# Performance work log

Hardware: AMD Instinct MI355X
Metric: run time of the kernel (lower is better)

The kernel has to match this reference:

```python
import jax, jax.numpy as jnp
import numpy as np

ALPHA = 1.0  # args.alpha
BS, N_HIDDEN, N_CLUSTERS = 1048576, 64, 64


def setup_inputs() -> dict:
    key = jax.random.key(0)
    k1, k2 = jax.random.split(key)
    z = jax.random.normal(k1, (BS, N_HIDDEN), dtype=jnp.float32)
    centroids = jax.random.normal(k2, (N_CLUSTERS, N_HIDDEN), dtype=jnp.float32)
    return {"z": z, "centroids": centroids}


def reference(z, centroids):
    # EUC similarity: sim[b,k] = sqrt(sum_h (z[b,h] - c[k,h])^2)
    # computed via ||z||^2 + ||c||^2 - 2 z c^T (same math, no (K,bs,H) blowup)
    z2 = jnp.sum(z * z, axis=1, keepdims=True)            # (bs, 1)
    c2 = jnp.sum(centroids * centroids, axis=1)           # (K,)
    d2 = z2 + c2[None, :] - 2.0 * (z @ centroids.T)       # (bs, K)
    sim = jnp.sqrt(jnp.maximum(d2, 0.0))

    # Student-t soft assignment Q and target distribution P
    Q = (1.0 + sim / ALPHA) ** (-(ALPHA + 1.0) / 2.0)
    Q = Q / jnp.sum(Q, axis=1, keepdims=True)             # row-normalize
    P = (Q * Q) / jnp.sum(Q, axis=0, keepdims=True)       # col-sum sharpen
    P = P / jnp.sum(P, axis=1, keepdims=True)             # row-normalize
    return Q, P
```

## Files before the change

### kernel.cpp

```cpp
#include <hip/hip_runtime.h>

#define BS_N 1048576
#define NH 64
#define NK 64

#define WS_C2_OFF 512

__device__ __forceinline__ float frcp(float x) { return __builtin_amdgcn_rcpf(x); }

__global__ void k0_init(const float* __restrict__ c, float* __restrict__ ws) {
    const int t = threadIdx.x;
    for (int i = t; i < 512; i += 128) ws[i] = 0.f;
    if (t < 64) {
        const float* row = c + t * NH;
        float s0 = 0.f, s1 = 0.f, s2 = 0.f, s3 = 0.f;
#pragma unroll
        for (int h = 0; h < NH; h += 4) {
            s0 = fmaf(row[h + 0], row[h + 0], s0);
            s1 = fmaf(row[h + 1], row[h + 1], s1);
            s2 = fmaf(row[h + 2], row[h + 2], s2);
            s3 = fmaf(row[h + 3], row[h + 3], s3);
        }
        ws[WS_C2_OFF + t] = (s0 + s1) + (s2 + s3);
    }
}

__global__ __launch_bounds__(128) void k1_q(const float* __restrict__ z,
                                            const float* __restrict__ c,
                                            float* __restrict__ ws,
                                            float* __restrict__ Q) {
    __shared__ float qs[128 * 65];
    __shared__ float rs[128];
    __shared__ float cpart[2][64];
    const int t = threadIdx.x;
    const long long row = (long long)blockIdx.x * 128 + t;
    const float* __restrict__ c2p = ws + WS_C2_OFF;
    float* colsum = ws + (size_t)(blockIdx.x & 7) * 64;

    const float4* z4 = reinterpret_cast<const float4*>(z) + row * 16;
    float zr[NH];
#pragma unroll
    for (int i = 0; i < 16; i++) {
        float4 v = z4[i];
        zr[4 * i + 0] = v.x; zr[4 * i + 1] = v.y;
        zr[4 * i + 2] = v.z; zr[4 * i + 3] = v.w;
    }
    float z20 = 0.f, z21 = 0.f, z22 = 0.f, z23 = 0.f;
#pragma unroll
    for (int h = 0; h < NH; h += 4) {
        z20 = fmaf(zr[h + 0], zr[h + 0], z20);
        z21 = fmaf(zr[h + 1], zr[h + 1], z21);
        z22 = fmaf(zr[h + 2], zr[h + 2], z22);
        z23 = fmaf(zr[h + 3], zr[h + 3], z23);
    }
    const float z2 = (z20 + z21) + (z22 + z23);

    float rowsum = 0.f;
    for (int k = 0; k < NK; k++) {
        const float4* c4 = reinterpret_cast<const float4*>(c) + k * 16;
        float a0 = 0.f, a1 = 0.f, a2 = 0.f, a3 = 0.f;
#pragma unroll
        for (int i = 0; i < 16; i++) {
            float4 cv = c4[i];
            a0 = fmaf(zr[4 * i + 0], cv.x, a0);
            a1 = fmaf(zr[4 * i + 1], cv.y, a1);
            a2 = fmaf(zr[4 * i + 2], cv.z, a2);
            a3 = fmaf(zr[4 * i + 3], cv.w, a3);
        }
        const float dot = (a0 + a1) + (a2 + a3);
        float d2 = z2 + c2p[k] - 2.f * dot;
        d2 = fmaxf(d2, 0.f);
        const float sim = sqrtf(d2);
        const float qu = frcp(1.f + sim);
        rowsum += qu;
        qs[t * 65 + k] = qu;
    }
    const float rinv = frcp(rowsum);
    rs[t] = rinv;
    __syncthreads();

    float4* Q4 = reinterpret_cast<float4*>(Q) + row * 16;
#pragma unroll
    for (int i = 0; i < 16; i++) {
        float4 v;
        v.x = qs[t * 65 + 4 * i + 0] * rinv;
        v.y = qs[t * 65 + 4 * i + 1] * rinv;
        v.z = qs[t * 65 + 4 * i + 2] * rinv;
        v.w = qs[t * 65 + 4 * i + 3] * rinv;
        Q4[i] = v;
    }

    const int k = t & 63, g = t >> 6;
    float s = 0.f;
#pragma unroll 8
    for (int r = 0; r < 64; r++) {
        const int rr = g * 64 + r;
        s = fmaf(qs[rr * 65 + k], rs[rr], s);
    }
    cpart[g][k] = s;
    __syncthreads();
    if (t < 64) atomicAdd(&colsum[t], cpart[0][t] + cpart[1][t]);
}

__global__ __launch_bounds__(256) void k2_p(const float* __restrict__ ws,
                                            const float* __restrict__ Q,
                                            float* __restrict__ P) {
    __shared__ __align__(16) float rcs[64];
    const int t = threadIdx.x;
    if (t < 64) {
        float s = 0.f;
#pragma unroll
        for (int rep = 0; rep < 8; rep++) s += ws[rep * 64 + t];
        rcs[t] = frcp(s);
    }
    __syncthreads();

    const long long row = (long long)(gridDim.x - 1 - blockIdx.x) * 256 + t;
    const float4* Q4 = reinterpret_cast<const float4*>(Q) + row * 16;
    float4* P4 = reinterpret_cast<float4*>(P) + row * 16;

    float pu[NK];
    float s0 = 0.f, s1 = 0.f, s2 = 0.f, s3 = 0.f;
#pragma unroll
    for (int i = 0; i < 16; i++) {
        float4 v = Q4[i];
        float4 cc = *reinterpret_cast<const float4*>(&rcs[4 * i]);
        pu[4 * i + 0] = v.x * v.x * cc.x; s0 += pu[4 * i + 0];
        pu[4 * i + 1] = v.y * v.y * cc.y; s1 += pu[4 * i + 1];
        pu[4 * i + 2] = v.z * v.z * cc.z; s2 += pu[4 * i + 2];
        pu[4 * i + 3] = v.w * v.w * cc.w; s3 += pu[4 * i + 3];
    }
    const float rinv = frcp((s0 + s1) + (s2 + s3));
#pragma unroll
    for (int i = 0; i < 16; i++) {
        float4 o;
        o.x = pu[4 * i + 0] * rinv;
        o.y = pu[4 * i + 1] * rinv;
        o.z = pu[4 * i + 2] * rinv;
        o.w = pu[4 * i + 3] * rinv;
        P4[i] = o;
    }
}

extern "C" void kernel_launch(void* const* d_in, const int* in_sizes, int n_in,
                              void* d_out, int out_size, void* d_ws, size_t ws_size,
                              hipStream_t stream) {
    const float* z = (const float*)d_in[0];
    const float* c = (const float*)d_in[1];
    float* Q = (float*)d_out;
    float* P = (float*)d_out + (size_t)BS_N * NK;
    float* ws = (float*)d_ws;

    k0_init<<<1, 128, 0, stream>>>(c, ws);
    k1_q<<<BS_N / 128, 128, 0, stream>>>(z, c, ws, Q);
    k2_p<<<BS_N / 256, 256, 0, stream>>>(ws, Q, P);
}
```

Baseline: 912.6 us.

## Replace shared-memory column reduction with register butterfly shuffles in Q kernel

Q values stay in registers instead of being staged in a large padded shared-memory tile, and the per-block column sums are computed with a recursive-halving butterfly of wavefront shuffles, followed by one atomic per lane per wavefront. The block size doubles to 256 threads and the distance loop is fully unrolled. This removes the shared-memory footprint and barriers that limited occupancy. In exchange it adds register pressure from holding 64 z values plus 64 q values per thread, and four times as many atomics onto the same eight colsum slots.

```diff
diff --git a/kernel.cpp b/kernel.cpp
--- a/kernel.cpp
+++ b/kernel.cpp
@@ -25,19 +25,16 @@
     }
 }
 
-__global__ __launch_bounds__(128) void k1_q(const float* __restrict__ z,
+__global__ __launch_bounds__(256) void k1_q(const float* __restrict__ z,
                                             const float* __restrict__ c,
-                                            float* __restrict__ ws,
+                                            const float* __restrict__ c2p,
+                                            float* __restrict__ colsum_base,
                                             float* __restrict__ Q) {
-    __shared__ float qs[128 * 65];
-    __shared__ float rs[128];
-    __shared__ float cpart[2][64];
     const int t = threadIdx.x;
-    const long long row = (long long)blockIdx.x * 128 + t;
-    const float* __restrict__ c2p = ws + WS_C2_OFF;
-    float* colsum = ws + (size_t)(blockIdx.x & 7) * 64;
+    const int lane = t & 63;
+    const long long row = (long long)blockIdx.x * 256 + t;
 
-    const float4* z4 = reinterpret_cast<const float4*>(z) + row * 16;
+    const float4* __restrict__ z4 = reinterpret_cast<const float4*>(z) + row * 16;
     float zr[NH];
 #pragma unroll
     for (int i = 0; i < 16; i++) {
@@ -55,13 +52,14 @@
     }
     const float z2 = (z20 + z21) + (z22 + z23);
 
-    float rowsum = 0.f;
+    float qu[NK];
+    const float4* __restrict__ c4 = reinterpret_cast<const float4*>(c);
+#pragma unroll
     for (int k = 0; k < NK; k++) {
-        const float4* c4 = reinterpret_cast<const float4*>(c) + k * 16;
         float a0 = 0.f, a1 = 0.f, a2 = 0.f, a3 = 0.f;
 #pragma unroll
         for (int i = 0; i < 16; i++) {
-            float4 cv = c4[i];
+            const float4 cv = c4[k * 16 + i];
             a0 = fmaf(zr[4 * i + 0], cv.x, a0);
             a1 = fmaf(zr[4 * i + 1], cv.y, a1);
             a2 = fmaf(zr[4 * i + 2], cv.z, a2);
@@ -71,35 +69,43 @@
         float d2 = z2 + c2p[k] - 2.f * dot;
         d2 = fmaxf(d2, 0.f);
         const float sim = sqrtf(d2);
-        const float qu = frcp(1.f + sim);
-        rowsum += qu;
-        qs[t * 65 + k] = qu;
+        qu[k] = frcp(1.f + sim);
     }
-    const float rinv = frcp(rowsum);
-    rs[t] = rinv;
-    __syncthreads();
 
-    float4* Q4 = reinterpret_cast<float4*>(Q) + row * 16;
+    float rs0 = 0.f, rs1 = 0.f, rs2 = 0.f, rs3 = 0.f;
+#pragma unroll
+    for (int k = 0; k < NK; k += 4) {
+        rs0 += qu[k + 0]; rs1 += qu[k + 1];
+        rs2 += qu[k + 2]; rs3 += qu[k + 3];
+    }
+    const float rinv = frcp((rs0 + rs1) + (rs2 + rs3));
+
+    float4* __restrict__ Q4 = reinterpret_cast<float4*>(Q) + row * 16;
 #pragma unroll
     for (int i = 0; i < 16; i++) {
-        float4 v;
-        v.x = qs[t * 65 + 4 * i + 0] * rinv;
-        v.y = qs[t * 65 + 4 * i + 1] * rinv;
-        v.z = qs[t * 65 + 4 * i + 2] * rinv;
-        v.w = qs[t * 65 + 4 * i + 3] * rinv;
-        Q4[i] = v;
+        float4 o;
+        o.x = qu[4 * i + 0] * rinv;
+        o.y = qu[4 * i + 1] * rinv;
+        o.z = qu[4 * i + 2] * rinv;
+        o.w = qu[4 * i + 3] * rinv;
+        qu[4 * i + 0] = o.x; qu[4 * i + 1] = o.y;
+        qu[4 * i + 2] = o.z; qu[4 * i + 3] = o.w;
+        Q4[i] = o;
     }
 
-    const int k = t & 63, g = t >> 6;
-    float s = 0.f;
-#pragma unroll 8
-    for (int r = 0; r < 64; r++) {
-        const int rr = g * 64 + r;
-        s = fmaf(qs[rr * 65 + k], rs[rr], s);
+#pragma unroll
+    for (int r = 0; r < 6; r++) {
+        const int n = NK >> (r + 1);
+        const bool hi = (lane >> r) & 1;
+#pragma unroll
+        for (int i = 0; i < n; i++) {
+            const float mine = hi ? qu[2 * i + 1] : qu[2 * i];
+            const float oth  = hi ? qu[2 * i]     : qu[2 * i + 1];
+            qu[i] = mine + __shfl_xor(oth, 1 << r, 64);
+        }
     }
-    cpart[g][k] = s;
-    __syncthreads();
-    if (t < 64) atomicAdd(&colsum[t], cpart[0][t] + cpart[1][t]);
+    float* colsum = colsum_base + (size_t)(blockIdx.x & 7) * 64;
+    atomicAdd(&colsum[lane], qu[0]);
 }
 
 __global__ __launch_bounds__(256) void k2_p(const float* __restrict__ ws,
@@ -152,6 +158,6 @@
     float* ws = (float*)d_ws;
 
     k0_init<<<1, 128, 0, stream>>>(c, ws);
-    k1_q<<<BS_N / 128, 128, 0, stream>>>(z, c, ws, Q);
+    k1_q<<<BS_N / 256, 256, 0, stream>>>(z, c, ws + WS_C2_OFF, ws, Q);
     k2_p<<<BS_N / 256, 256, 0, stream>>>(ws, Q, P);
 }
```

New measurement: 931.0 us. 1.02x slower.
